# Optimization experiments

Hardware: AMD Instinct MI355X
Metric: run time of the kernel (lower is better)

The kernel has to match this reference:

```python
import jax, jax.numpy as jnp
import numpy as np

N = 100000       # nodes
E = 3200000      # edges (avg degree 32)
NFEAT, NHID, NCLASS = 256, 128, 40


def setup_inputs() -> dict:
    key = jax.random.key(0)
    ks = jax.random.split(key, 6)
    x = jax.random.normal(ks[0], (N, NFEAT), jnp.float32)
    edge_rows = jax.random.randint(ks[1], (E,), 0, N)   # destination nodes
    edge_cols = jax.random.randint(ks[2], (E,), 0, N)   # source nodes
    # SageConv proj: Linear(2*in, out, bias=False); weight stored [out, in] torch-style
    W1 = jax.random.normal(ks[3], (NHID, 2 * NFEAT), jnp.float32) * 0.05
    W2 = jax.random.normal(ks[4], (NHID, 2 * NHID), jnp.float32) * 0.05
    mlp_W = jax.random.normal(ks[5], (NCLASS, NHID), jnp.float32) * 0.05  # init.normal_(std=0.05)
    mlp_b = jnp.zeros((NCLASS,), jnp.float32)
    return {"x": x, "W1": W1, "W2": W2, "mlp_W": mlp_W, "mlp_b": mlp_b,
            "edge_rows": edge_rows, "edge_cols": edge_cols}


def _sage_conv(h, W, rows, cols, deg):
    # neigh = spmm(adj, h) / (deg + 1); adj binary COO (rows <- cols)
    neigh = jax.ops.segment_sum(h[cols], rows, num_segments=N) / (deg + 1.0)[:, None]
    return jnp.concatenate([h, neigh], axis=-1) @ W.T


def reference(x, W1, W2, mlp_W, mlp_b, edge_rows, edge_cols):
    deg = jax.ops.segment_sum(jnp.ones((E,), x.dtype), edge_rows, num_segments=N)
    h = jax.nn.relu(_sage_conv(x, W1, edge_rows, edge_cols, deg))   # dropout: eval no-op
    h = jax.nn.relu(_sage_conv(h, W2, edge_rows, edge_cols, deg))
    logits = h @ mlp_W.T + mlp_b
    return jax.nn.log_softmax(logits, axis=1)
```

## Files before the change

kernel.cpp:

```cpp
#include <hip/hip_runtime.h>
#include <hip/hip_bf16.h>

#define NFEAT 256
#define NHID  128
#define NCLASS 40

typedef __attribute__((ext_vector_type(8))) short short8;
typedef __attribute__((ext_vector_type(4))) float float4v;

__device__ __forceinline__ unsigned short f2bf(float f) {
    union { float f; unsigned u; } v; v.f = f;
    unsigned r = v.u + 0x7fff + ((v.u >> 16) & 1);
    return (unsigned short)(r >> 16);
}
__device__ __forceinline__ float bflo(unsigned u) { return __uint_as_float(u << 16); }
__device__ __forceinline__ float bfhi(unsigned u) { return __uint_as_float(u & 0xffff0000u); }
__device__ __forceinline__ unsigned cvtpk_bf16(float a, float b) {
    unsigned r;
    asm("v_cvt_pk_bf16_f32 %0, %1, %2" : "=v"(r) : "v"(a), "v"(b));
    return r;
}

__device__ __forceinline__ void ld_g2l16(const unsigned short* gp, unsigned short* lp) {
    __builtin_amdgcn_global_load_lds((const __attribute__((address_space(1))) unsigned short*)gp,
                                     (__attribute__((address_space(3))) unsigned short*)lp,
                                     16, 0, 0);
}

#define TILE_E 4096
#define WCAP   20480

__global__ __launch_bounds__(256) void prep_fused(const int* __restrict__ rows,
                                                  const int* __restrict__ cols,
                                                  int* __restrict__ gcur,
                                                  unsigned* __restrict__ binned, int E, int nbuck,
                                                  int nblk,
                                                  const float* __restrict__ W1,
                                                  const float* __restrict__ W2,
                                                  const float* __restrict__ Wm,
                                                  unsigned short* __restrict__ Wp1,
                                                  unsigned short* __restrict__ Wp2,
                                                  unsigned short* __restrict__ Wb) {
    int t = threadIdx.x;
    if ((int)blockIdx.x >= nblk) {
        int b = blockIdx.x - nblk;
        if (b < 256) {
            float v = (b < 128) ? W1[b * 512 + t] : W1[(b - 128) * 512 + 256 + t];
            Wp1[(size_t)(t >> 5) * 256 * 32 + b * 32 + (t & 31)] = f2bf(v);
        } else if (b < 512) {
            int o = b - 256;
            if (t < 128) {
                float v = (o < 128) ? W2[o * 256 + t] : W2[(o - 128) * 256 + 128 + t];
                Wp2[(size_t)(t >> 5) * 256 * 32 + o * 32 + (t & 31)] = f2bf(v);
            }
        } else {
            int o = b - 512;
            if (t < 128) Wb[o * 128 + t] = (o < NCLASS) ? f2bf(Wm[o * 128 + t]) : 0;
        }
        return;
    }
    __shared__ int hh[256];
    __shared__ int lbase[256];
    __shared__ int lcur[256];
    hh[t] = 0;
    __syncthreads();
    int e0 = blockIdx.x * TILE_E;
    int4 rv[4];
    #pragma unroll
    for (int it = 0; it < TILE_E / 1024; ++it) {
        int base = e0 + (it * 256 + t) * 4;
        if (base + 3 < E) {
            rv[it] = *reinterpret_cast<const int4*>(&rows[base]);
            atomicAdd(&hh[rv[it].x >> 9], 1);
            atomicAdd(&hh[rv[it].y >> 9], 1);
            atomicAdd(&hh[rv[it].z >> 9], 1);
            atomicAdd(&hh[rv[it].w >> 9], 1);
        } else {
            for (int k = 0; k < 4; ++k)
                if (base + k < E) atomicAdd(&hh[rows[base + k] >> 9], 1);
        }
    }
    __syncthreads();
    if (t < nbuck) {
        int h = hh[t];
        lbase[t] = t * WCAP + (h ? atomicAdd(&gcur[t], h) : 0);
        lcur[t] = 0;
    }
    __syncthreads();
    #pragma unroll
    for (int it = 0; it < TILE_E / 1024; ++it) {
        int base = e0 + (it * 256 + t) * 4;
        if (base + 3 < E) {
            int4 r = rv[it];
            int4 c = *reinterpret_cast<const int4*>(&cols[base]);
            int b0 = r.x >> 9, b1 = r.y >> 9, b2 = r.z >> 9, b3 = r.w >> 9;
            int d0 = lbase[b0] + atomicAdd(&lcur[b0], 1);
            int d1 = lbase[b1] + atomicAdd(&lcur[b1], 1);
            int d2 = lbase[b2] + atomicAdd(&lcur[b2], 1);
            int d3 = lbase[b3] + atomicAdd(&lcur[b3], 1);
            binned[d0] = ((unsigned)(r.x & 511) << 17) | (unsigned)c.x;
            binned[d1] = ((unsigned)(r.y & 511) << 17) | (unsigned)c.y;
            binned[d2] = ((unsigned)(r.z & 511) << 17) | (unsigned)c.z;
            binned[d3] = ((unsigned)(r.w & 511) << 17) | (unsigned)c.w;
        } else {
            for (int k = 0; k < 4; ++k)
                if (base + k < E) {
                    int r = rows[base + k];
                    int b = r >> 9;
                    int dst = lbase[b] + atomicAdd(&lcur[b], 1);
                    binned[dst] = ((unsigned)(r & 511) << 17) | (unsigned)cols[base + k];
                }
        }
    }
}

__global__ __launch_bounds__(512) void gemm1_fw(const float* __restrict__ X,
                                                const unsigned short* __restrict__ Wp,
                                                unsigned short* __restrict__ PS,
                                                unsigned char* __restrict__ PN8,
                                                int M, int nfw,
                                                const unsigned* __restrict__ binned,
                                                const int* __restrict__ gcur,
                                                int4* __restrict__ rpd,
                                                int* __restrict__ csr_cols, int N) {
    __shared__ __align__(16) char smem[24576];
    const int t = threadIdx.x;

    if ((int)blockIdx.x < nfw) {
        int* h    = (int*)smem;
        int* ps   = h + 512;
        int* lcur = ps + 256;
        int w = blockIdx.x;
        int r0 = w << 9;
        h[t] = 0;
        if (t < 256) ps[t] = 0;
        __syncthreads();
        int beg = w * WCAP, end = beg + gcur[w];
        for (int e = beg + t; e < end; e += 512)
            atomicAdd(&h[binned[e] >> 17], 1);
        __syncthreads();
        int pair = 0;
        if (t < 256) { pair = h[2 * t] + h[2 * t + 1]; ps[t] = pair; }
        __syncthreads();
        for (int off = 1; off < 256; off <<= 1) {
            int tmp = (t >= off && t < 256) ? ps[t - off] : 0;
            __syncthreads();
            if (t < 256) ps[t] += tmp;
            __syncthreads();
        }
        if (t < 256) {
            int base0 = beg + ps[t] - pair;
            int base1 = base0 + h[2 * t];
            int r_a = r0 + 2 * t, r_b = r0 + 2 * t + 1;
            if (r_a < N) {
                int4 m; m.x = base0; m.y = h[2 * t];
                m.z = __float_as_int(1.0f / ((float)h[2 * t] + 1.0f)); m.w = 0;
                rpd[r_a] = m;
            }
            if (r_b < N) {
                int4 m; m.x = base1; m.y = h[2 * t + 1];
                m.z = __float_as_int(1.0f / ((float)h[2 * t + 1] + 1.0f)); m.w = 0;
                rpd[r_b] = m;
            }
            lcur[2 * t] = base0;
            lcur[2 * t + 1] = base1;
        }
        __syncthreads();
        for (int e = beg + t; e < end; e += 512) {
            unsigned v = binned[e];
            int idx = atomicAdd(&lcur[v >> 17], 1);
            csr_cols[idx] = (int)(v & 0x1FFFFu);
        }
        return;
    }

    unsigned short* sA = (unsigned short*)smem;
    unsigned short* sB = (unsigned short*)(smem + 8192);
    const int lane = t & 63;
    const int wave = t >> 6;
    const int m0 = (blockIdx.x - nfw) * 128;
    const int wm = (wave >> 2) * 64;
    const int wn = (wave & 3) * 64;

    const int r15 = lane & 15;
    const int k8  = (lane >> 4) * 8;
    const int arow = t >> 2;
    const int ac8  = (t & 3) * 8;
    const int brow = lane >> 2;
    const int bc8  = (lane & 3) * 8;

    float4v acc[4][4] = {{{0.f,0.f,0.f,0.f}}};
    const int gm = min(m0 + arow, M - 1);
    const float* gA = X + (size_t)gm * 256 + ac8;

    for (int k0 = 0; k0 < 256; k0 += 32) {
        const unsigned short* pan = Wp + (size_t)(k0 >> 5) * 256 * 32;
        float4 v0 = *reinterpret_cast<const float4*>(gA + k0);
        float4 v1 = *reinterpret_cast<const float4*>(gA + k0 + 4);
        uint4 q;
        q.x = cvtpk_bf16(v0.x, v0.y);
        q.y = cvtpk_bf16(v0.z, v0.w);
        q.z = cvtpk_bf16(v1.x, v1.y);
        q.w = cvtpk_bf16(v1.z, v1.w);
        *reinterpret_cast<uint4*>(&sA[arow * 32 + ac8]) = q;
        #pragma unroll
        for (int it = 0; it < 2; ++it) {
            int slab = it * 128 + wave * 16;
            ld_g2l16(pan + (size_t)(slab + brow) * 32 + bc8, &sB[slab * 32]);
        }
        __syncthreads();

        short8 aF[4], bF[4];
        #pragma unroll
        for (int i = 0; i < 4; ++i)
            aF[i] = *reinterpret_cast<const short8*>(&sA[(wm + i * 16 + r15) * 32 + k8]);
        #pragma unroll
        for (int j = 0; j < 4; ++j)
            bF[j] = *reinterpret_cast<const short8*>(&sB[(wn + j * 16 + r15) * 32 + k8]);
        #pragma unroll
        for (int i = 0; i < 4; ++i)
            #pragma unroll
            for (int j = 0; j < 4; ++j)
                acc[i][j] = __builtin_amdgcn_mfma_f32_16x16x32_bf16(aF[i], bF[j], acc[i][j], 0, 0, 0);
        __syncthreads();
    }

    #pragma unroll
    for (int i = 0; i < 4; ++i) {
        #pragma unroll
        for (int r = 0; r < 4; ++r) {
            int row = m0 + wm + i * 16 + (lane >> 4) * 4 + r;
            #pragma unroll
            for (int j = 0; j < 4; ++j) {
                float v  = acc[i][j][r];
                float vn = __shfl_xor(v, 1);
                int cN = wn + j * 16 + r15;
                if (row < M && !(r15 & 1)) {
                    if (cN < 128) {
                        *reinterpret_cast<unsigned*>(&PS[(size_t)row * 128 + cN]) = cvtpk_bf16(v, vn);
                    } else {
                        unsigned p8 = __builtin_amdgcn_cvt_pk_fp8_f32(v, vn, 0u, false);
                        *reinterpret_cast<unsigned short*>(&PN8[(size_t)row * 128 + (cN - 128)]) =
                            (unsigned short)p8;
                    }
                }
            }
        }
    }
}

__global__ __launch_bounds__(512) void gemm2_mfma(const unsigned short* __restrict__ H,
                                                  const unsigned short* __restrict__ Wp,
                                                  unsigned short* __restrict__ PS,
                                                  unsigned char* __restrict__ PN8,
                                                  int M) {
    __shared__ unsigned short sA[128 * 32];
    __shared__ unsigned short sB[256 * 32];
    const int t    = threadIdx.x;
    const int lane = t & 63;
    const int wave = t >> 6;
    const int m0 = blockIdx.x * 128;
    const int wm = (wave >> 2) * 64;
    const int wn = (wave & 3) * 64;

    const int r15 = lane & 15;
    const int k8  = (lane >> 4) * 8;
    const int brow = lane >> 2;
    const int bc8  = (lane & 3) * 8;

    float4v acc[4][4] = {{{0.f,0.f,0.f,0.f}}};

    for (int k0 = 0; k0 < 128; k0 += 32) {
        const unsigned short* pan = Wp + (size_t)(k0 >> 5) * 256 * 32;
        int slabA = wave * 16;
        ld_g2l16(H + (size_t)(m0 + slabA + brow) * 128 + k0 + bc8, &sA[slabA * 32]);
        #pragma unroll
        for (int it = 0; it < 2; ++it) {
            int slab = it * 128 + wave * 16;
            ld_g2l16(pan + (size_t)(slab + brow) * 32 + bc8, &sB[slab * 32]);
        }
        __syncthreads();

        short8 aF[4], bF[4];
        #pragma unroll
        for (int i = 0; i < 4; ++i)
            aF[i] = *reinterpret_cast<const short8*>(&sA[(wm + i * 16 + r15) * 32 + k8]);
        #pragma unroll
        for (int j = 0; j < 4; ++j)
            bF[j] = *reinterpret_cast<const short8*>(&sB[(wn + j * 16 + r15) * 32 + k8]);
        #pragma unroll
        for (int i = 0; i < 4; ++i)
            #pragma unroll
            for (int j = 0; j < 4; ++j)
                acc[i][j] = __builtin_amdgcn_mfma_f32_16x16x32_bf16(aF[i], bF[j], acc[i][j], 0, 0, 0);
        __syncthreads();
    }

    #pragma unroll
    for (int i = 0; i < 4; ++i) {
        #pragma unroll
        for (int r = 0; r < 4; ++r) {
            int row = m0 + wm + i * 16 + (lane >> 4) * 4 + r;
            #pragma unroll
            for (int j = 0; j < 4; ++j) {
                float v  = acc[i][j][r];
                float vn = __shfl_xor(v, 1);
                int cN = wn + j * 16 + r15;
                if (row < M && !(r15 & 1)) {
                    if (cN < 128) {
                        *reinterpret_cast<unsigned*>(&PS[(size_t)row * 128 + cN]) = cvtpk_bf16(v, vn);
                    } else {
                        unsigned p8 = __builtin_amdgcn_cvt_pk_fp8_f32(v, vn, 0u, false);
                        *reinterpret_cast<unsigned short*>(&PN8[(size_t)row * 128 + (cN - 128)]) =
                            (unsigned short)p8;
                    }
                }
            }
        }
    }
}

__device__ __forceinline__ void acc_fp8x8(uint2 u,
                                          float& a0, float& a1, float& a2, float& a3,
                                          float& a4, float& a5, float& a6, float& a7) {
    auto f01 = __builtin_amdgcn_cvt_pk_f32_fp8(u.x, false);
    auto f23 = __builtin_amdgcn_cvt_pk_f32_fp8(u.x, true);
    auto f45 = __builtin_amdgcn_cvt_pk_f32_fp8(u.y, false);
    auto f67 = __builtin_amdgcn_cvt_pk_f32_fp8(u.y, true);
    a0 += f01[0]; a1 += f01[1]; a2 += f23[0]; a3 += f23[1];
    a4 += f45[0]; a5 += f45[1]; a6 += f67[0]; a7 += f67[1];
}

__global__ __launch_bounds__(256) void gather_combine(const unsigned short* __restrict__ PS,
                                                      const unsigned char* __restrict__ PN8,
                                                      const int4* __restrict__ rpd,
                                                      const int* __restrict__ csr_cols,
                                                      unsigned short* __restrict__ H, int N) {
    int node = (blockIdx.x * blockDim.x + threadIdx.x) >> 6;
    if (node >= N) return;
    int lane = threadIdx.x & 63;
    int grp  = lane >> 4;
    int l16  = lane & 15;
    int4 md = rpd[node];
    int beg = md.x, end = md.x + md.y;
    float id = __int_as_float(md.z);

    uint4 us = {0u, 0u, 0u, 0u};
    if (grp == 0)
        us = *reinterpret_cast<const uint4*>(&PS[(size_t)node * 128 + l16 * 8]);

    float a0=0,a1=0,a2=0,a3=0,a4=0,a5=0,a6=0,a7=0;
    int p0 = beg + grp;
    for (; p0 + 12 < end; p0 += 16) {
        int cA = csr_cols[p0];
        int cB = csr_cols[p0 + 4];
        int cC = csr_cols[p0 + 8];
        int cD = csr_cols[p0 + 12];
        uint2 uA = *reinterpret_cast<const uint2*>(&PN8[(size_t)cA * 128 + l16 * 8]);
        uint2 uB = *reinterpret_cast<const uint2*>(&PN8[(size_t)cB * 128 + l16 * 8]);
        uint2 uC = *reinterpret_cast<const uint2*>(&PN8[(size_t)cC * 128 + l16 * 8]);
        uint2 uD = *reinterpret_cast<const uint2*>(&PN8[(size_t)cD * 128 + l16 * 8]);
        acc_fp8x8(uA, a0, a1, a2, a3, a4, a5, a6, a7);
        acc_fp8x8(uB, a0, a1, a2, a3, a4, a5, a6, a7);
        acc_fp8x8(uC, a0, a1, a2, a3, a4, a5, a6, a7);
        acc_fp8x8(uD, a0, a1, a2, a3, a4, a5, a6, a7);
    }
    for (; p0 < end; p0 += 4) {
        int c = csr_cols[p0];
        uint2 u = *reinterpret_cast<const uint2*>(&PN8[(size_t)c * 128 + l16 * 8]);
        acc_fp8x8(u, a0, a1, a2, a3, a4, a5, a6, a7);
    }
    a0 += __shfl_xor(a0, 16); a1 += __shfl_xor(a1, 16);
    a2 += __shfl_xor(a2, 16); a3 += __shfl_xor(a3, 16);
    a4 += __shfl_xor(a4, 16); a5 += __shfl_xor(a5, 16);
    a6 += __shfl_xor(a6, 16); a7 += __shfl_xor(a7, 16);
    a0 += __shfl_xor(a0, 32); a1 += __shfl_xor(a1, 32);
    a2 += __shfl_xor(a2, 32); a3 += __shfl_xor(a3, 32);
    a4 += __shfl_xor(a4, 32); a5 += __shfl_xor(a5, 32);
    a6 += __shfl_xor(a6, 32); a7 += __shfl_xor(a7, 32);

    if (grp == 0) {
        float h0 = fmaxf(fmaf(a0, id, bflo(us.x)), 0.f);
        float h1 = fmaxf(fmaf(a1, id, bfhi(us.x)), 0.f);
        float h2 = fmaxf(fmaf(a2, id, bflo(us.y)), 0.f);
        float h3 = fmaxf(fmaf(a3, id, bfhi(us.y)), 0.f);
        float h4 = fmaxf(fmaf(a4, id, bflo(us.z)), 0.f);
        float h5 = fmaxf(fmaf(a5, id, bfhi(us.z)), 0.f);
        float h6 = fmaxf(fmaf(a6, id, bflo(us.w)), 0.f);
        float h7 = fmaxf(fmaf(a7, id, bfhi(us.w)), 0.f);
        uint4 o;
        o.x = cvtpk_bf16(h0, h1); o.y = cvtpk_bf16(h2, h3);
        o.z = cvtpk_bf16(h4, h5); o.w = cvtpk_bf16(h6, h7);
        *reinterpret_cast<uint4*>(&H[(size_t)node * 128 + l16 * 8]) = o;
    }
}

__global__ __launch_bounds__(256) void mlp_head_mfma(const unsigned short* __restrict__ H,
                                                     const unsigned short* __restrict__ Wb,
                                                     const float* __restrict__ bm,
                                                     float* __restrict__ out, int N) {
    __shared__ unsigned short sW[48 * 128];
    int t = threadIdx.x;
    for (int i = t; i < 48 * 128 / 2; i += 256)
        ((unsigned*)sW)[i] = ((const unsigned*)Wb)[i];
    __syncthreads();

    const int wave = t >> 6, lane = t & 63;
    const int m0 = blockIdx.x * 64 + wave * 16;
    if (m0 >= N) return;
    const int r15 = lane & 15;
    const int k8  = (lane >> 4) * 8;
    const int arow = min(m0 + r15, N - 1);

    float4v acc[3] = {{0.f,0.f,0.f,0.f},{0.f,0.f,0.f,0.f},{0.f,0.f,0.f,0.f}};
    #pragma unroll
    for (int k0 = 0; k0 < 128; k0 += 32) {
        short8 a = *reinterpret_cast<const short8*>(&H[(size_t)arow * 128 + k0 + k8]);
        #pragma unroll
        for (int f = 0; f < 3; ++f) {
            short8 b = *reinterpret_cast<const short8*>(&sW[(f * 16 + r15) * 128 + k0 + k8]);
            acc[f] = __builtin_amdgcn_mfma_f32_16x16x32_bf16(a, b, acc[f], 0, 0, 0);
        }
    }

    float bias[3]; bool cv[3];
    #pragma unroll
    for (int f = 0; f < 3; ++f) {
        int c = f * 16 + r15;
        cv[f] = (c < NCLASS);
        bias[f] = cv[f] ? bm[c] : 0.f;
    }
    #pragma unroll
    for (int r = 0; r < 4; ++r) {
        int node = m0 + (lane >> 4) * 4 + r;
        float lg[3];
        float m = -1e30f;
        #pragma unroll
        for (int f = 0; f < 3; ++f) {
            lg[f] = cv[f] ? (acc[f][r] + bias[f]) : -1e30f;
            m = fmaxf(m, lg[f]);
        }
        m = fmaxf(m, __shfl_xor(m, 1));
        m = fmaxf(m, __shfl_xor(m, 2));
        m = fmaxf(m, __shfl_xor(m, 4));
        m = fmaxf(m, __shfl_xor(m, 8));
        float s = 0.f;
        #pragma unroll
        for (int f = 0; f < 3; ++f) s += cv[f] ? __expf(lg[f] - m) : 0.f;
        s += __shfl_xor(s, 1);
        s += __shfl_xor(s, 2);
        s += __shfl_xor(s, 4);
        s += __shfl_xor(s, 8);
        float ls = __logf(s);
        if (node < N) {
            #pragma unroll
            for (int f = 0; f < 3; ++f)
                if (cv[f]) out[(size_t)node * NCLASS + f * 16 + r15] = lg[f] - m - ls;
        }
    }
}

extern "C" void kernel_launch(void* const* d_in, const int* in_sizes, int n_in,
                              void* d_out, int out_size, void* d_ws, size_t ws_size,
                              hipStream_t stream) {
    const float* x    = (const float*)d_in[0];
    const float* W1   = (const float*)d_in[1];
    const float* W2   = (const float*)d_in[2];
    const float* mlpW = (const float*)d_in[3];
    const float* mlpb = (const float*)d_in[4];
    const int*   rows = (const int*)d_in[5];
    const int*   cols = (const int*)d_in[6];

    const int N = in_sizes[0] / NFEAT;
    const int E = in_sizes[5];

    char* ws = (char*)d_ws;
    size_t off = 0;
    auto alloc = [&](size_t bytes) -> void* {
        void* p = ws + off;
        off = (off + bytes + 255) & ~(size_t)255;
        return p;
    };
    const int nbuck = (N + 511) >> 9;
    const int nblk  = (E + TILE_E - 1) / TILE_E;

    unsigned short* PS  = (unsigned short*)alloc((size_t)N * 128 * 2);
    unsigned char*  PN8 = (unsigned char*) alloc((size_t)N * 128);
    unsigned short* H   = (unsigned short*)alloc((size_t)N * 128 * 2);
    int4*  RPD    = (int4*) alloc((size_t)N * 16);
    int*   CSRC   = (int*)  alloc((size_t)nbuck * WCAP * 4);
    unsigned* BINNED = (unsigned*)alloc((size_t)nbuck * WCAP * 4);
    int*   GCUR   = (int*)  alloc((size_t)256 * 4);
    unsigned short* Wp1 = (unsigned short*)alloc((size_t)256 * 256 * 2);
    unsigned short* Wp2 = (unsigned short*)alloc((size_t)128 * 256 * 2);
    unsigned short* Wb  = (unsigned short*)alloc((size_t)48 * 128 * 2);

    const int mblocks = (N + 127) / 128;
    const int gblocks = (int)(((long long)N * 64 + 255) / 256);

    hipMemsetAsync(GCUR, 0, 256 * 4, stream);
    prep_fused<<<nblk + 560, 256, 0, stream>>>(rows, cols, GCUR, BINNED, E, nbuck, nblk,
                                               W1, W2, mlpW, Wp1, Wp2, Wb);

    gemm1_fw<<<nbuck + mblocks, 512, 0, stream>>>(x, Wp1, PS, PN8, N, nbuck,
                                                  BINNED, GCUR, RPD, CSRC, N);
    gather_combine<<<gblocks, 256, 0, stream>>>(PS, PN8, RPD, CSRC, H, N);

    gemm2_mfma<<<mblocks, 512, 0, stream>>>(H, Wp2, PS, PN8, N);
    gather_combine<<<gblocks, 256, 0, stream>>>(PS, PN8, RPD, CSRC, H, N);

    mlp_head_mfma<<<(N + 63) / 64, 256, 0, stream>>>(H, Wb, mlpb, (float*)d_out, N);
}
```

Measured before the change: 418.7 us.

## Double-buffer LDS tiles and XOR-swizzle layouts in both MFMA GEMM kernels

Both GEMM kernels now use two LDS buffers per operand and issue the next K-slice loads before the MFMAs on the current slice. That removes one barrier per iteration and overlaps global loads with compute. Weights are pre-packed, and A tiles are stored, with an XOR swizzle on 8-element chunks to cut LDS bank conflicts on fragment reads. LDS per block doubles to 48KB, which may lower occupancy, and the single barrier per iteration relies on the buffer alternation being correct.

```diff
diff --git a/kernel.cpp b/kernel.cpp
--- a/kernel.cpp
+++ b/kernel.cpp
@@ -29,6 +29,7 @@
 
 #define TILE_E 4096
 #define WCAP   20480
+
 
 __global__ __launch_bounds__(256) void prep_fused(const int* __restrict__ rows,
                                                   const int* __restrict__ cols,
@@ -46,12 +47,14 @@
         int b = blockIdx.x - nblk;
         if (b < 256) {
             float v = (b < 128) ? W1[b * 512 + t] : W1[(b - 128) * 512 + 256 + t];
-            Wp1[(size_t)(t >> 5) * 256 * 32 + b * 32 + (t & 31)] = f2bf(v);
+            Wp1[(size_t)(t >> 5) * 8192 + b * 32 +
+                ((((t >> 3) & 3) ^ (b & 3)) << 3) + (t & 7)] = f2bf(v);
         } else if (b < 512) {
             int o = b - 256;
             if (t < 128) {
                 float v = (o < 128) ? W2[o * 256 + t] : W2[(o - 128) * 256 + 128 + t];
-                Wp2[(size_t)(t >> 5) * 256 * 32 + o * 32 + (t & 31)] = f2bf(v);
+                Wp2[(size_t)(t >> 5) * 8192 + o * 32 +
+                    ((((t >> 3) & 3) ^ (o & 3)) << 3) + (t & 7)] = f2bf(v);
             }
         } else {
             int o = b - 512;
@@ -123,7 +126,7 @@
                                                 const int* __restrict__ gcur,
                                                 int4* __restrict__ rpd,
                                                 int* __restrict__ csr_cols, int N) {
-    __shared__ __align__(16) char smem[24576];
+    __shared__ __align__(16) char smem[49152];
     const int t = threadIdx.x;
 
     if ((int)blockIdx.x < nfw) {
@@ -174,8 +177,10 @@
         return;
     }
 
-    unsigned short* sA = (unsigned short*)smem;
-    unsigned short* sB = (unsigned short*)(smem + 8192);
+    unsigned short* const sA0 = (unsigned short*)smem;
+    unsigned short* const sA1 = (unsigned short*)(smem + 8192);
+    unsigned short* const sB0 = (unsigned short*)(smem + 16384);
+    unsigned short* const sB1 = (unsigned short*)(smem + 32768);
     const int lane = t & 63;
     const int wave = t >> 6;
     const int m0 = (blockIdx.x - nfw) * 128;
@@ -183,46 +188,66 @@
     const int wn = (wave & 3) * 64;
 
     const int r15 = lane & 15;
-    const int k8  = (lane >> 4) * 8;
+    const int kx8 = (((lane >> 4) ^ (r15 & 3))) * 8;
     const int arow = t >> 2;
-    const int ac8  = (t & 3) * 8;
+    const int awz  = (((t & 3) ^ (arow & 3))) * 8;
     const int brow = lane >> 2;
     const int bc8  = (lane & 3) * 8;
 
     float4v acc[4][4] = {{{0.f,0.f,0.f,0.f}}};
     const int gm = min(m0 + arow, M - 1);
-    const float* gA = X + (size_t)gm * 256 + ac8;
-
-    for (int k0 = 0; k0 < 256; k0 += 32) {
-        const unsigned short* pan = Wp + (size_t)(k0 >> 5) * 256 * 32;
-        float4 v0 = *reinterpret_cast<const float4*>(gA + k0);
-        float4 v1 = *reinterpret_cast<const float4*>(gA + k0 + 4);
+    const float* gA = X + (size_t)gm * 256 + (t & 3) * 8;
+
+    {
+        float4 v0 = *reinterpret_cast<const float4*>(gA);
+        float4 v1 = *reinterpret_cast<const float4*>(gA + 4);
         uint4 q;
-        q.x = cvtpk_bf16(v0.x, v0.y);
-        q.y = cvtpk_bf16(v0.z, v0.w);
-        q.z = cvtpk_bf16(v1.x, v1.y);
-        q.w = cvtpk_bf16(v1.z, v1.w);
-        *reinterpret_cast<uint4*>(&sA[arow * 32 + ac8]) = q;
+        q.x = cvtpk_bf16(v0.x, v0.y); q.y = cvtpk_bf16(v0.z, v0.w);
+        q.z = cvtpk_bf16(v1.x, v1.y); q.w = cvtpk_bf16(v1.z, v1.w);
+        *reinterpret_cast<uint4*>(&sA0[arow * 32 + awz]) = q;
         #pragma unroll
         for (int it = 0; it < 2; ++it) {
             int slab = it * 128 + wave * 16;
-            ld_g2l16(pan + (size_t)(slab + brow) * 32 + bc8, &sB[slab * 32]);
-        }
+            ld_g2l16(Wp + (size_t)(slab + brow) * 32 + bc8, &sB0[slab * 32]);
+        }
+    }
+
+    #pragma unroll
+    for (int k = 0; k < 8; ++k) {
+        unsigned short* const sAc = (k & 1) ? sA1 : sA0;
+        unsigned short* const sBc = (k & 1) ? sB1 : sB0;
+        unsigned short* const sAn = (k & 1) ? sA0 : sA1;
+        unsigned short* const sBn = (k & 1) ? sB0 : sB1;
         __syncthreads();
-
+        float4 vx0, vx1;
+        if (k < 7) {
+            const unsigned short* pan = Wp + (size_t)(k + 1) * 8192;
+            #pragma unroll
+            for (int it = 0; it < 2; ++it) {
+                int slab = it * 128 + wave * 16;
+                ld_g2l16(pan + (size_t)(slab + brow) * 32 + bc8, &sBn[slab * 32]);
+            }
+            vx0 = *reinterpret_cast<const float4*>(gA + (k + 1) * 32);
+            vx1 = *reinterpret_cast<const float4*>(gA + (k + 1) * 32 + 4);
+        }
         short8 aF[4], bF[4];
         #pragma unroll
         for (int i = 0; i < 4; ++i)
-            aF[i] = *reinterpret_cast<const short8*>(&sA[(wm + i * 16 + r15) * 32 + k8]);
+            aF[i] = *reinterpret_cast<const short8*>(&sAc[(wm + i * 16 + r15) * 32 + kx8]);
         #pragma unroll
         for (int j = 0; j < 4; ++j)
-            bF[j] = *reinterpret_cast<const short8*>(&sB[(wn + j * 16 + r15) * 32 + k8]);
+            bF[j] = *reinterpret_cast<const short8*>(&sBc[(wn + j * 16 + r15) * 32 + kx8]);
         #pragma unroll
         for (int i = 0; i < 4; ++i)
             #pragma unroll
             for (int j = 0; j < 4; ++j)
                 acc[i][j] = __builtin_amdgcn_mfma_f32_16x16x32_bf16(aF[i], bF[j], acc[i][j], 0, 0, 0);
-        __syncthreads();
+        if (k < 7) {
+            uint4 q;
+            q.x = cvtpk_bf16(vx0.x, vx0.y); q.y = cvtpk_bf16(vx0.z, vx0.w);
+            q.z = cvtpk_bf16(vx1.x, vx1.y); q.w = cvtpk_bf16(vx1.z, vx1.w);
+            *reinterpret_cast<uint4*>(&sAn[arow * 32 + awz]) = q;
+        }
     }
 
     #pragma unroll
@@ -254,8 +279,11 @@
                                                   unsigned short* __restrict__ PS,
                                                   unsigned char* __restrict__ PN8,
                                                   int M) {
-    __shared__ unsigned short sA[128 * 32];
-    __shared__ unsigned short sB[256 * 32];
+    __shared__ __align__(16) char smem[49152];
+    unsigned short* const sA0 = (unsigned short*)smem;
+    unsigned short* const sA1 = (unsigned short*)(smem + 8192);
+    unsigned short* const sB0 = (unsigned short*)(smem + 16384);
+    unsigned short* const sB1 = (unsigned short*)(smem + 32768);
     const int t    = threadIdx.x;
     const int lane = t & 63;
     const int wave = t >> 6;
@@ -264,36 +292,50 @@
     const int wn = (wave & 3) * 64;
 
     const int r15 = lane & 15;
-    const int k8  = (lane >> 4) * 8;
+    const int kx8 = (((lane >> 4) ^ (r15 & 3))) * 8;
     const int brow = lane >> 2;
     const int bc8  = (lane & 3) * 8;
+    const int hswz = (((lane & 3) ^ (brow & 3))) * 8;
 
     float4v acc[4][4] = {{{0.f,0.f,0.f,0.f}}};
-
-    for (int k0 = 0; k0 < 128; k0 += 32) {
-        const unsigned short* pan = Wp + (size_t)(k0 >> 5) * 256 * 32;
-        int slabA = wave * 16;
-        ld_g2l16(H + (size_t)(m0 + slabA + brow) * 128 + k0 + bc8, &sA[slabA * 32]);
-        #pragma unroll
-        for (int it = 0; it < 2; ++it) {
-            int slab = it * 128 + wave * 16;
-            ld_g2l16(pan + (size_t)(slab + brow) * 32 + bc8, &sB[slab * 32]);
-        }
+    const int slabA = wave * 16;
+    const unsigned short* gH = H + (size_t)(m0 + slabA + brow) * 128 + hswz;
+
+    ld_g2l16(gH, &sA0[slabA * 32]);
+    #pragma unroll
+    for (int it = 0; it < 2; ++it) {
+        int slab = it * 128 + wave * 16;
+        ld_g2l16(Wp + (size_t)(slab + brow) * 32 + bc8, &sB0[slab * 32]);
+    }
+
+    #pragma unroll
+    for (int k = 0; k < 4; ++k) {
+        unsigned short* const sAc = (k & 1) ? sA1 : sA0;
+        unsigned short* const sBc = (k & 1) ? sB1 : sB0;
+        unsigned short* const sAn = (k & 1) ? sA0 : sA1;
+        unsigned short* const sBn = (k & 1) ? sB0 : sB1;
         __syncthreads();
-
+        if (k < 3) {
+            ld_g2l16(gH + (k + 1) * 32, &sAn[slabA * 32]);
+            const unsigned short* pan = Wp + (size_t)(k + 1) * 8192;
+            #pragma unroll
+            for (int it = 0; it < 2; ++it) {
+                int slab = it * 128 + wave * 16;
+                ld_g2l16(pan + (size_t)(slab + brow) * 32 + bc8, &sBn[slab * 32]);
+            }
+        }
         short8 aF[4], bF[4];
         #pragma unroll
         for (int i = 0; i < 4; ++i)
-            aF[i] = *reinterpret_cast<const short8*>(&sA[(wm + i * 16 + r15) * 32 + k8]);
+            aF[i] = *reinterpret_cast<const short8*>(&sAc[(wm + i * 16 + r15) * 32 + kx8]);
         #pragma unroll
         for (int j = 0; j < 4; ++j)
-            bF[j] = *reinterpret_cast<const short8*>(&sB[(wn + j * 16 + r15) * 32 + k8]);
+            bF[j] = *reinterpret_cast<const short8*>(&sBc[(wn + j * 16 + r15) * 32 + kx8]);
         #pragma unroll
         for (int i = 0; i < 4; ++i)
             #pragma unroll
             for (int j = 0; j < 4; ++j)
                 acc[i][j] = __builtin_amdgcn_mfma_f32_16x16x32_bf16(aF[i], bF[j], acc[i][j], 0, 0, 0);
-        __syncthreads();
     }
 
     #pragma unroll
```

New measurement: 419.5 us. About the same (+0.2%).

## Pre-convert X to swizzled bf16 and load full A tiles via LDS DMA

Applied to the files above, without the earlier changes.

Adds a bf16 conversion of X to the prep kernel and writes it in an XOR-swizzled layout. Both GEMMs now load the whole 128-row A tile into LDS at once with global_load_lds, which removes the per-k-step barriers. B fragments are read straight from global memory instead of being staged in LDS. H is also written swizzled so gemm2 and the MLP head read it without bank conflicts. The cost is an extra 51 MB bf16 round trip for X and 64 KB of LDS in gemm1, which limits occupancy.

```diff
diff --git a/kernel.cpp b/kernel.cpp
--- a/kernel.cpp
+++ b/kernel.cpp
@@ -29,6 +29,7 @@
 
 #define TILE_E 4096
 #define WCAP   20480
+
 
 __global__ __launch_bounds__(256) void prep_fused(const int* __restrict__ rows,
                                                   const int* __restrict__ cols,
@@ -40,18 +41,37 @@
                                                   const float* __restrict__ Wm,
                                                   unsigned short* __restrict__ Wp1,
                                                   unsigned short* __restrict__ Wp2,
-                                                  unsigned short* __restrict__ Wb) {
+                                                  unsigned short* __restrict__ Wb,
+                                                  const float* __restrict__ X,
+                                                  unsigned short* __restrict__ X16, int N) {
     int t = threadIdx.x;
+    if ((int)blockIdx.x >= nblk + 560) {
+        int idx0 = (blockIdx.x - nblk - 560) * 2048;
+        #pragma unroll
+        for (int it = 0; it < 8; ++it) {
+            int idx = idx0 + it * 256 + t;
+            int r = idx >> 5, u = idx & 31;
+            if (r < N) {
+                const float4* px = reinterpret_cast<const float4*>(X + (size_t)r * 256 + u * 8);
+                float4 v0 = px[0], v1 = px[1];
+                uint4 q;
+                q.x = cvtpk_bf16(v0.x, v0.y); q.y = cvtpk_bf16(v0.z, v0.w);
+                q.z = cvtpk_bf16(v1.x, v1.y); q.w = cvtpk_bf16(v1.z, v1.w);
+                *reinterpret_cast<uint4*>(&X16[(size_t)r * 256 + ((u ^ (r & 7)) * 8)]) = q;
+            }
+        }
+        return;
+    }
     if ((int)blockIdx.x >= nblk) {
         int b = blockIdx.x - nblk;
         if (b < 256) {
             float v = (b < 128) ? W1[b * 512 + t] : W1[(b - 128) * 512 + 256 + t];
-            Wp1[(size_t)(t >> 5) * 256 * 32 + b * 32 + (t & 31)] = f2bf(v);
+            Wp1[(size_t)(t >> 5) * 8192 + b * 32 + (t & 31)] = f2bf(v);
         } else if (b < 512) {
             int o = b - 256;
             if (t < 128) {
                 float v = (o < 128) ? W2[o * 256 + t] : W2[(o - 128) * 256 + 128 + t];
-                Wp2[(size_t)(t >> 5) * 256 * 32 + o * 32 + (t & 31)] = f2bf(v);
+                Wp2[(size_t)(t >> 5) * 8192 + o * 32 + (t & 31)] = f2bf(v);
             }
         } else {
             int o = b - 512;
@@ -114,7 +134,7 @@
     }
 }
 
-__global__ __launch_bounds__(512) void gemm1_fw(const float* __restrict__ X,
+__global__ __launch_bounds__(512) void gemm1_fw(const unsigned short* __restrict__ X16,
                                                 const unsigned short* __restrict__ Wp,
                                                 unsigned short* __restrict__ PS,
                                                 unsigned char* __restrict__ PN8,
@@ -123,7 +143,7 @@
                                                 const int* __restrict__ gcur,
                                                 int4* __restrict__ rpd,
                                                 int* __restrict__ csr_cols, int N) {
-    __shared__ __align__(16) char smem[24576];
+    __shared__ __align__(16) char smem[65536];
     const int t = threadIdx.x;
 
     if ((int)blockIdx.x < nfw) {
@@ -174,55 +194,45 @@
         return;
     }
 
-    unsigned short* sA = (unsigned short*)smem;
-    unsigned short* sB = (unsigned short*)(smem + 8192);
+    unsigned short* const sA = (unsigned short*)smem;
     const int lane = t & 63;
     const int wave = t >> 6;
     const int m0 = (blockIdx.x - nfw) * 128;
     const int wm = (wave >> 2) * 64;
     const int wn = (wave & 3) * 64;
-
     const int r15 = lane & 15;
-    const int k8  = (lane >> 4) * 8;
-    const int arow = t >> 2;
-    const int ac8  = (t & 3) * 8;
-    const int brow = lane >> 2;
-    const int bc8  = (lane & 3) * 8;
+    const int l4  = lane >> 4;
+
+    #pragma unroll
+    for (int it = 0; it < 8; ++it) {
+        int row = it * 16 + (t >> 5);
+        int gm  = min(m0 + row, M - 1);
+        ld_g2l16(X16 + (size_t)gm * 256 + (t & 31) * 8,
+                 (unsigned short*)(smem + it * 8192 + wave * 1024));
+    }
+    __syncthreads();
 
     float4v acc[4][4] = {{{0.f,0.f,0.f,0.f}}};
-    const int gm = min(m0 + arow, M - 1);
-    const float* gA = X + (size_t)gm * 256 + ac8;
-
-    for (int k0 = 0; k0 < 256; k0 += 32) {
-        const unsigned short* pan = Wp + (size_t)(k0 >> 5) * 256 * 32;
-        float4 v0 = *reinterpret_cast<const float4*>(gA + k0);
-        float4 v1 = *reinterpret_cast<const float4*>(gA + k0 + 4);
-        uint4 q;
-        q.x = cvtpk_bf16(v0.x, v0.y);
-        q.y = cvtpk_bf16(v0.z, v0.w);
-        q.z = cvtpk_bf16(v1.x, v1.y);
-        q.w = cvtpk_bf16(v1.z, v1.w);
-        *reinterpret_cast<uint4*>(&sA[arow * 32 + ac8]) = q;
-        #pragma unroll
-        for (int it = 0; it < 2; ++it) {
-            int slab = it * 128 + wave * 16;
-            ld_g2l16(pan + (size_t)(slab + brow) * 32 + bc8, &sB[slab * 32]);
-        }
-        __syncthreads();
-
+    #pragma unroll
+    for (int k = 0; k < 8; ++k) {
         short8 aF[4], bF[4];
         #pragma unroll
-        for (int i = 0; i < 4; ++i)
-            aF[i] = *reinterpret_cast<const short8*>(&sA[(wm + i * 16 + r15) * 32 + k8]);
-        #pragma unroll
-        for (int j = 0; j < 4; ++j)
-            bF[j] = *reinterpret_cast<const short8*>(&sB[(wn + j * 16 + r15) * 32 + k8]);
+        for (int i = 0; i < 4; ++i) {
+            int row  = wm + i * 16 + r15;
+            int koct = k * 4 + l4;
+            int u    = koct ^ (row & 7);
+            aF[i] = *reinterpret_cast<const short8*>(&sA[row * 256 + u * 8]);
+        }
+        #pragma unroll
+        for (int j = 0; j < 4; ++j) {
+            int o = wn + j * 16 + r15;
+            bF[j] = *reinterpret_cast<const short8*>(&Wp[(size_t)k * 8192 + o * 32 + l4 * 8]);
+        }
         #pragma unroll
         for (int i = 0; i < 4; ++i)
             #pragma unroll
             for (int j = 0; j < 4; ++j)
                 acc[i][j] = __builtin_amdgcn_mfma_f32_16x16x32_bf16(aF[i], bF[j], acc[i][j], 0, 0, 0);
-        __syncthreads();
     }
 
     #pragma unroll
@@ -254,46 +264,45 @@
                                                   unsigned short* __restrict__ PS,
                                                   unsigned char* __restrict__ PN8,
                                                   int M) {
-    __shared__ unsigned short sA[128 * 32];
-    __shared__ unsigned short sB[256 * 32];
+    __shared__ __align__(16) unsigned short sA[128 * 128];
     const int t    = threadIdx.x;
     const int lane = t & 63;
     const int wave = t >> 6;
     const int m0 = blockIdx.x * 128;
     const int wm = (wave >> 2) * 64;
     const int wn = (wave & 3) * 64;
-
     const int r15 = lane & 15;
-    const int k8  = (lane >> 4) * 8;
-    const int brow = lane >> 2;
-    const int bc8  = (lane & 3) * 8;
+    const int l4  = lane >> 4;
+
+    #pragma unroll
+    for (int it = 0; it < 4; ++it) {
+        int row = it * 32 + (t >> 4);
+        ld_g2l16(H + (size_t)(m0 + row) * 128 + (t & 15) * 8,
+                 (unsigned short*)((char*)sA + it * 8192 + wave * 1024));
+    }
+    __syncthreads();
 
     float4v acc[4][4] = {{{0.f,0.f,0.f,0.f}}};
-
-    for (int k0 = 0; k0 < 128; k0 += 32) {
-        const unsigned short* pan = Wp + (size_t)(k0 >> 5) * 256 * 32;
-        int slabA = wave * 16;
-        ld_g2l16(H + (size_t)(m0 + slabA + brow) * 128 + k0 + bc8, &sA[slabA * 32]);
-        #pragma unroll
-        for (int it = 0; it < 2; ++it) {
-            int slab = it * 128 + wave * 16;
-            ld_g2l16(pan + (size_t)(slab + brow) * 32 + bc8, &sB[slab * 32]);
-        }
-        __syncthreads();
-
+    #pragma unroll
+    for (int k = 0; k < 4; ++k) {
         short8 aF[4], bF[4];
         #pragma unroll
-        for (int i = 0; i < 4; ++i)
-            aF[i] = *reinterpret_cast<const short8*>(&sA[(wm + i * 16 + r15) * 32 + k8]);
-        #pragma unroll
-        for (int j = 0; j < 4; ++j)
-            bF[j] = *reinterpret_cast<const short8*>(&sB[(wn + j * 16 + r15) * 32 + k8]);
+        for (int i = 0; i < 4; ++i) {
+            int row  = wm + i * 16 + r15;
+            int koct = k * 4 + l4;
+            int u    = koct ^ (row & 7);
+            aF[i] = *reinterpret_cast<const short8*>(&sA[row * 128 + u * 8]);
+        }
+        #pragma unroll
+        for (int j = 0; j < 4; ++j) {
+            int o = wn + j * 16 + r15;
+            bF[j] = *reinterpret_cast<const short8*>(&Wp[(size_t)k * 8192 + o * 32 + l4 * 8]);
+        }
         #pragma unroll
         for (int i = 0; i < 4; ++i)
             #pragma unroll
             for (int j = 0; j < 4; ++j)
                 acc[i][j] = __builtin_amdgcn_mfma_f32_16x16x32_bf16(aF[i], bF[j], acc[i][j], 0, 0, 0);
-        __syncthreads();
     }
 
     #pragma unroll
@@ -391,7 +400,7 @@
         uint4 o;
         o.x = cvtpk_bf16(h0, h1); o.y = cvtpk_bf16(h2, h3);
         o.z = cvtpk_bf16(h4, h5); o.w = cvtpk_bf16(h6, h7);
-        *reinterpret_cast<uint4*>(&H[(size_t)node * 128 + l16 * 8]) = o;
+        *reinterpret_cast<uint4*>(&H[(size_t)node * 128 + ((l16 ^ (node & 7)) * 8)]) = o;
     }
 }
 
@@ -415,7 +424,8 @@
     float4v acc[3] = {{0.f,0.f,0.f,0.f},{0.f,0.f,0.f,0.f},{0.f,0.f,0.f,0.f}};
     #pragma unroll
     for (int k0 = 0; k0 < 128; k0 += 32) {
-        short8 a = *reinterpret_cast<const short8*>(&H[(size_t)arow * 128 + k0 + k8]);
+        int u = (k0 >> 3) + (lane >> 4);
+        short8 a = *reinterpret_cast<const short8*>(&H[(size_t)arow * 128 + ((u ^ (arow & 7)) * 8)]);
         #pragma unroll
         for (int f = 0; f < 3; ++f) {
             short8 b = *reinterpret_cast<const short8*>(&sW[(f * 16 + r15) * 128 + k0 + k8]);
@@ -487,6 +497,7 @@
     unsigned short* PS  = (unsigned short*)alloc((size_t)N * 128 * 2);
     unsigned char*  PN8 = (unsigned char*) alloc((size_t)N * 128);
     unsigned short* H   = (unsigned short*)alloc((size_t)N * 128 * 2);
+    unsigned short* X16 = (unsigned short*)alloc((size_t)N * 256 * 2);
     int4*  RPD    = (int4*) alloc((size_t)N * 16);
     int*   CSRC   = (int*)  alloc((size_t)nbuck * WCAP * 4);
     unsigned* BINNED = (unsigned*)alloc((size_t)nbuck * WCAP * 4);
@@ -497,12 +508,13 @@
 
     const int mblocks = (N + 127) / 128;
     const int gblocks = (int)(((long long)N * 64 + 255) / 256);
+    const int ncvt    = (N * 32 + 2047) / 2048;
 
     hipMemsetAsync(GCUR, 0, 256 * 4, stream);
-    prep_fused<<<nblk + 560, 256, 0, stream>>>(rows, cols, GCUR, BINNED, E, nbuck, nblk,
-                                               W1, W2, mlpW, Wp1, Wp2, Wb);
-
-    gemm1_fw<<<nbuck + mblocks, 512, 0, stream>>>(x, Wp1, PS, PN8, N, nbuck,
+    prep_fused<<<nblk + 560 + ncvt, 256, 0, stream>>>(rows, cols, GCUR, BINNED, E, nbuck, nblk,
+                                                      W1, W2, mlpW, Wp1, Wp2, Wb, x, X16, N);
+
+    gemm1_fw<<<nbuck + mblocks, 512, 0, stream>>>(X16, Wp1, PS, PN8, N, nbuck,
                                                   BINNED, GCUR, RPD, CSRC, N);
     gather_combine<<<gblocks, 256, 0, stream>>>(PS, PN8, RPD, CSRC, H, N);
 
```

Result: slower. 431.7 us (+3.1%).
